# Performance work log

Measured on AMD Instinct MI355X. Metric: run time of the kernel, lower is better.

## Reference

```python
import jax, jax.numpy as jnp
import numpy as np

NEG_INF = -1e32

def _linear(x, W, b):
    # torch nn.Linear: x @ W.T + b
    return x @ W.T + b

def setup_inputs() -> dict:
    key = jax.random.key(0)
    B, T, D, H = 8, 1024, 512, 8
    ks = jax.random.split(key, 16)
    def rn(i, shape, scale=1.0):
        return jax.random.normal(ks[i], shape, dtype=jnp.float32) * scale
    W_SCALE = 0.04  # ~xavier for 512x512
    inp = {
        'q_mean': rn(0, (B, T, D)), 'q_cov': rn(1, (B, T, D)),
        'k_mean': rn(2, (B, T, D)), 'k_cov': rn(3, (B, T, D)),
        'v_mean': rn(4, (B, T, D)), 'v_cov': rn(5, (B, T, D)),
        # kq_same=True: q projections share k weights
        'Wk_mean': rn(6, (D, D), W_SCALE), 'bk_mean': jnp.zeros((D,), jnp.float32),
        'Wk_cov':  rn(7, (D, D), W_SCALE), 'bk_cov':  jnp.zeros((D,), jnp.float32),
        'Wv_mean': rn(8, (D, D), W_SCALE), 'bv_mean': jnp.zeros((D,), jnp.float32),
        'Wv_cov':  rn(9, (D, D), W_SCALE), 'bv_cov':  jnp.zeros((D,), jnp.float32),
        'Wo_mean': rn(10, (D, D), W_SCALE), 'bo_mean': jnp.zeros((D,), jnp.float32),
        'Wo_cov':  rn(11, (D, D), W_SCALE), 'bo_cov':  jnp.zeros((D,), jnp.float32),
        'gammas': rn(12, (H, 1, 1), 0.3),
        'mask': jnp.broadcast_to(jnp.tril(jnp.ones((T, T), dtype=bool))[None, None], (B, 1, T, T)),
        'zero_pad': 1,
    }
    return inp

def reference(q_mean, q_cov, k_mean, k_cov, v_mean, v_cov,
              Wk_mean, bk_mean, Wk_cov, bk_cov,
              Wv_mean, bv_mean, Wv_cov, bv_cov,
              Wo_mean, bo_mean, Wo_cov, bo_cov,
              gammas, mask, zero_pad):
    B, T, D = q_mean.shape
    H = gammas.shape[0]
    dk = D // H
    def split(x):  # (B,T,D) -> (B,H,T,dk)
        return x.reshape(B, T, H, dk).transpose(0, 2, 1, 3)
    km = split(_linear(k_mean, Wk_mean, bk_mean))
    kc = split(_linear(k_cov,  Wk_cov,  bk_cov))
    qm = split(_linear(q_mean, Wk_mean, bk_mean))  # kq_same
    qc = split(_linear(q_cov,  Wk_cov,  bk_cov))
    vm = split(_linear(v_mean, Wv_mean, bv_mean))
    vc = split(_linear(v_cov,  Wv_cov,  bv_cov))

    # Wasserstein distance (B,H,T,T)
    m1sq = jnp.sum(qm ** 2, -1, keepdims=True)
    m2sq = jnp.sum(km ** 2, -1, keepdims=True)
    ret = -2.0 * jnp.einsum('bhtd,bhsd->bhts', qm, km) + m1sq + jnp.swapaxes(m2sq, -1, -2)
    sq_q = jnp.sqrt(jnp.clip(qc, 1e-24))
    sq_k = jnp.sqrt(jnp.clip(kc, 1e-24))
    cov_ret = (-2.0 * jnp.einsum('bhtd,bhsd->bhts', sq_q, sq_k)
               + jnp.sum(qc, -1, keepdims=True)
               + jnp.swapaxes(jnp.sum(kc, -1, keepdims=True), -1, -2))
    scores = -(ret + cov_ret) / jnp.sqrt(jnp.float32(dk))

    # cumulative position-decay term (no-grad block in torch)
    s_ = jnp.where(mask, scores, NEG_INF)
    s_ = jax.nn.softmax(s_, axis=-1) * mask.astype(scores.dtype)
    distcum = jnp.cumsum(s_, axis=-1)
    disttot = jnp.sum(s_, axis=-1, keepdims=True)
    idx = jnp.arange(T)
    pos = jnp.abs(idx[None, :] - idx[:, None]).astype(jnp.float32)[None, None]  # (1,1,T,T)
    dist_scores = jax.lax.stop_gradient(jnp.sqrt(jnp.clip((disttot - distcum) * pos, 0.0)))

    gamma = -jax.nn.softplus(gammas)[None]  # (1,H,1,1)
    total_effect = jnp.clip(jnp.exp(dist_scores * gamma), 1e-5, 1e5)
    scores = jnp.where(mask, scores * total_effect, NEG_INF)
    scores = jax.nn.softmax(scores, axis=-1)
    if zero_pad:
        scores = scores.at[:, :, 0, :].set(0.0)
    # dropout is identity (p=0 / eval)

    out_mean = jnp.einsum('bhts,bhsd->bhtd', scores, vm)
    out_cov  = jnp.einsum('bhts,bhsd->bhtd', scores ** 2, vc)
    cm = out_mean.transpose(0, 2, 1, 3).reshape(B, T, D)
    cc = out_cov.transpose(0, 2, 1, 3).reshape(B, T, D)
    return (_linear(cm, Wo_mean, bo_mean), _linear(cc, Wo_cov, bo_cov))
```

## Files before the change

kernel.cpp:

```cpp
#include <hip/hip_runtime.h>
#include <hip/hip_bf16.h>
#include <hip/hip_fp16.h>

#define Bb 8
#define Tt 1024
#define Dd 512
#define Hh 8

typedef _Float16 half8 __attribute__((ext_vector_type(8)));
typedef float floatx4 __attribute__((ext_vector_type(4)));

__device__ __forceinline__ half8 cvt8(float4 a, float4 b) {
    half8 h;
    h[0] = (_Float16)a.x; h[1] = (_Float16)a.y; h[2] = (_Float16)a.z; h[3] = (_Float16)a.w;
    h[4] = (_Float16)b.x; h[5] = (_Float16)b.y; h[6] = (_Float16)b.z; h[7] = (_Float16)b.w;
    return h;
}

__device__ __forceinline__ void async16(const _Float16* g, _Float16* l) {
    __builtin_amdgcn_global_load_lds(
        (const __attribute__((address_space(1))) uint32_t*)g,
        (__attribute__((address_space(3))) uint32_t*)l, 16, 0, 0);
}

#define DPP_ADD(v, ctrl) \
    ((v) + __int_as_float(__builtin_amdgcn_update_dpp(0, __float_as_int(v), (ctrl), 0xF, 0xF, true)))

__device__ __forceinline__ float red16(float v) {
    v = DPP_ADD(v, 0xB1);
    v = DPP_ADD(v, 0x4E);
    v = DPP_ADD(v, 0x141);
    v = DPP_ADD(v, 0x140);
    return v;
}
__device__ __forceinline__ float scan16(float v) {
    v = DPP_ADD(v, 0x111);
    v = DPP_ADD(v, 0x112);
    v = DPP_ADD(v, 0x114);
    v = DPP_ADD(v, 0x118);
    return v;
}

__global__ __launch_bounds__(256) void cvt_pre(
    const float* __restrict__ s0, const float* __restrict__ s1,
    const float* __restrict__ s2, const float* __restrict__ s3,
    const float* __restrict__ s4, const float* __restrict__ s5,
    const float* __restrict__ w0, const float* __restrict__ w1,
    const float* __restrict__ w2, const float* __restrict__ w3,
    const float* __restrict__ w4, const float* __restrict__ w5,
    _Float16* __restrict__ dst)
{
    const size_t N_BTD = (size_t)Bb * Tt * Dd;
    const size_t NX = 6 * N_BTD;
    const size_t total8 = (NX + 6 * 262144) / 8;
    size_t i = (size_t)blockIdx.x * 256 + threadIdx.x;
    const size_t stride = (size_t)gridDim.x * 256;
    for (; i < total8; i += stride) {
        const size_t e = i * 8;
        const float* src;
        size_t off;
        if (e < NX) {
            const int seg = (int)(e >> 22);
            off = e & (N_BTD - 1);
            src = (seg == 0) ? s0 : (seg == 1) ? s1 : (seg == 2) ? s2
                : (seg == 3) ? s3 : (seg == 4) ? s4 : s5;
        } else {
            const size_t we = e - NX;
            const int seg = (int)(we >> 18);
            off = we & 262143;
            src = (seg == 0) ? w0 : (seg == 1) ? w1 : (seg == 2) ? w2
                : (seg == 3) ? w3 : (seg == 4) ? w4 : w5;
        }
        float4 a = *(const float4*)(src + off);
        float4 b = *(const float4*)(src + off + 4);
        *(half8*)(dst + e) = cvt8(a, b);
    }
}

template<bool TR>
__device__ __forceinline__ void gemm_tile_h(
    const _Float16* __restrict__ X, const _Float16* __restrict__ W,
    _Float16* As, _Float16* Bs, int m0, int n0, floatx4 acc[8])
{
    const int tid = threadIdx.x;
    const int w = tid >> 6, lane = tid & 63;
    const int sl = lane & 15, quad = lane >> 4;

    for (int k0 = 0; k0 < 512; k0 += 64) {
        __syncthreads();
        {
            const int r = tid >> 2;
            const int cb = (tid & 3) * 16;
            const _Float16* xp = X + (size_t)(m0 + r) * 512 + k0 + cb;
            *(uint4*)(As + r * 72 + cb)     = *(const uint4*)(xp);
            *(uint4*)(As + r * 72 + cb + 8) = *(const uint4*)(xp + 8);
        }
        {
            const int r = tid >> 1;
            const int cb = (tid & 1) * 32;
            const _Float16* wp = W + (size_t)(n0 + r) * 512 + k0 + cb;
            #pragma unroll
            for (int i = 0; i < 4; i++)
                *(uint4*)(Bs + r * 72 + cb + i * 8) = *(const uint4*)(wp + i * 8);
        }
        __syncthreads();
        #pragma unroll
        for (int kc = 0; kc < 64; kc += 32) {
            const half8 af = *(const half8*)(As + (w * 16 + sl) * 72 + kc + quad * 8);
            #pragma unroll
            for (int tn = 0; tn < 8; tn++) {
                const half8 bf = *(const half8*)(Bs + (tn * 16 + sl) * 72 + kc + quad * 8);
                if constexpr (TR)
                    acc[tn] = __builtin_amdgcn_mfma_f32_16x16x32_f16(bf, af, acc[tn], 0, 0, 0);
                else
                    acc[tn] = __builtin_amdgcn_mfma_f32_16x16x32_f16(af, bf, acc[tn], 0, 0, 0);
            }
        }
    }
}

__global__ __launch_bounds__(256) void gemm6(
    const _Float16* __restrict__ XH, const _Float16* __restrict__ WH,
    const float* __restrict__ bk_mean, const float* __restrict__ bk_cov,
    const float* __restrict__ bv_mean, const float* __restrict__ bv_cov,
    _Float16* __restrict__ QB, _Float16* __restrict__ KB, _Float16* __restrict__ VB,
    float* __restrict__ RROW, float* __restrict__ CCOL)
{
    __shared__ __align__(16) _Float16 As[64 * 72];
    __shared__ __align__(16) _Float16 Bs[128 * 72];

    const int f = blockIdx.x;
    const int work = (f & 7) * 384 + (f >> 3);
    const int z = work >> 9;
    const int rem = work & 511;
    const int m0 = (rem >> 2) * 64;
    const int n0 = (rem & 3) * 128;

    const size_t N_BTD = (size_t)Bb * Tt * Dd;
    const _Float16* X = XH + (size_t)z * N_BTD;
    const _Float16* W;
    const float* bias;
    _Float16* outH; float* sums;
    int off, sumsq, do_sqrt;
    switch (z) {
    case 0:  W=WH;            bias=bk_mean; outH=QB; sums=RROW;   off=0;  sumsq=1; do_sqrt=0; break;
    case 1:  W=WH+262144;     bias=bk_cov;  outH=QB; sums=RROW;   off=64; sumsq=0; do_sqrt=1; break;
    case 2:  W=WH;            bias=bk_mean; outH=KB; sums=CCOL;   off=0;  sumsq=1; do_sqrt=0; break;
    case 3:  W=WH+262144;     bias=bk_cov;  outH=KB; sums=CCOL;   off=64; sumsq=0; do_sqrt=1; break;
    case 4:  W=WH+2*262144;   bias=bv_mean; outH=VB; sums=nullptr;off=0;  sumsq=0; do_sqrt=0; break;
    default: W=WH+3*262144;   bias=bv_cov;  outH=VB; sums=nullptr;off=64; sumsq=0; do_sqrt=0; break;
    }

    floatx4 acc[8];
    #pragma unroll
    for (int tn = 0; tn < 8; tn++) acc[tn] = (floatx4){0.f, 0.f, 0.f, 0.f};

    const int tid = threadIdx.x;
    const int w = tid >> 6, lane = tid & 63;
    const int sl = lane & 15, quad = lane >> 4;

    if (z < 4) {
        gemm_tile_h<false>(X, W, As, Bs, m0, n0, acc);
        #pragma unroll
        for (int r = 0; r < 4; r++) {
            const int m = m0 + w * 16 + quad * 4 + r;
            const int b = m >> 10, t = m & 1023;
            float rs0 = 0.f, rs1 = 0.f;
            #pragma unroll
            for (int tn = 0; tn < 8; tn++) {
                const int n = n0 + tn * 16 + sl;
                const float v = acc[tn][r] + bias[n];
                if (tn < 4) rs0 += sumsq ? v * v : v;
                else        rs1 += sumsq ? v * v : v;
                const float sv = do_sqrt ? sqrtf(fmaxf(v, 1e-24f)) : v;
                const int head = n >> 6, dd = n & 63;
                outH[(((size_t)b * Hh + head) * Tt + t) * 128 + off + dd] = (_Float16)sv;
            }
            if (sums) {
                float v0 = rs0, v1 = rs1;
                v0 += __shfl_xor(v0, 1); v0 += __shfl_xor(v0, 2);
                v0 += __shfl_xor(v0, 4); v0 += __shfl_xor(v0, 8);
                v1 += __shfl_xor(v1, 1); v1 += __shfl_xor(v1, 2);
                v1 += __shfl_xor(v1, 4); v1 += __shfl_xor(v1, 8);
                if (sl == 0) {
                    atomicAdd(&sums[((size_t)b * Hh + (n0 >> 6) + 0) * Tt + t], v0);
                    atomicAdd(&sums[((size_t)b * Hh + (n0 >> 6) + 1) * Tt + t], v1);
                }
            }
        }
    } else {
        gemm_tile_h<true>(X, W, As, Bs, m0, n0, acc);
        const int m = m0 + w * 16 + sl;
        const int b = m >> 10, t = m & 1023;
        #pragma unroll
        for (int r = 0; r < 4; r++) {
            #pragma unroll
            for (int tn = 0; tn < 8; tn++) {
                const int n = n0 + tn * 16 + quad * 4 + r;
                const float v = acc[tn][r] + bias[n];
                const int head = n >> 6, dd = n & 63;
                outH[(((size_t)b * Hh + head) * 128 + off + dd) * 1024 + t] = (_Float16)v;
            }
        }
    }
}

__global__ __launch_bounds__(256) void gemm_out(
    const _Float16* __restrict__ CMh, const _Float16* __restrict__ CCh,
    const _Float16* __restrict__ WH,
    const float* __restrict__ bo_mean, const float* __restrict__ bo_cov,
    float* __restrict__ out, size_t outStride)
{
    __shared__ __align__(16) _Float16 As[64 * 72];
    __shared__ __align__(16) _Float16 Bs[128 * 72];

    const int f = blockIdx.x;
    const int work = (f & 7) * 128 + (f >> 3);
    const int z = work >> 9;
    const int rem = work & 511;
    const int m0 = (rem >> 2) * 64;
    const int n0 = (rem & 3) * 128;

    const _Float16* X = z ? CCh : CMh;
    const _Float16* W = WH + (size_t)(4 + z) * 262144;
    const float* bias = z ? bo_cov : bo_mean;
    float* outF       = out + (size_t)z * outStride;

    floatx4 acc[8];
    #pragma unroll
    for (int tn = 0; tn < 8; tn++) acc[tn] = (floatx4){0.f, 0.f, 0.f, 0.f};
    gemm_tile_h<false>(X, W, As, Bs, m0, n0, acc);

    const int tid = threadIdx.x;
    const int w = tid >> 6, lane = tid & 63;
    const int sl = lane & 15, quad = lane >> 4;

    #pragma unroll
    for (int r = 0; r < 4; r++) {
        const int m = m0 + w * 16 + quad * 4 + r;
        #pragma unroll
        for (int tn = 0; tn < 8; tn++) {
            const int n = n0 + tn * 16 + sl;
            outF[(size_t)m * 512 + n] = acc[tn][r] + bias[n];
        }
    }
}

__global__ __launch_bounds__(256) void attn_kernel(
    const _Float16* __restrict__ QB, const _Float16* __restrict__ KB,
    const _Float16* __restrict__ VBt, const float* __restrict__ RROW,
    const float* __restrict__ CCOL, const float* __restrict__ gammas,
    const int* __restrict__ zp, _Float16* __restrict__ CMh, _Float16* __restrict__ CCh)
{
    __shared__ __align__(16) _Float16 Vt[2][128 * 64];
    __shared__ __align__(16) _Float16 Pm[4][16 * 64];

    const int tid = threadIdx.x;
    const int g = blockIdx.x >> 6;
    const int bh = blockIdx.x & 63;
    const int rt = (g < 8) ? (15 - g) : (g - 8);
    const int t0 = rt * 64;
    const int h = bh & 7, b = bh >> 3;
    const int w = tid >> 6, lane = tid & 63;
    const int sl = lane & 15, quad = lane >> 4;
    const size_t rowbase = (size_t)bh * Tt;
    const int nch = rt + 1;

    const _Float16* VBb = VBt + (size_t)bh * 128 * 1024;
    const int vr8 = tid >> 3;
    const int vc8 = (tid & 7) << 3;
    const int vswz = (vr8 & 7) << 3;
    const _Float16* vsrc0 = VBb + (size_t)vr8 * 1024 + (vc8 ^ vswz);
    #define STAGE_V(cc, buf) do {                                          \
        const _Float16* _s = vsrc0 + (cc) * 64;                            \
        _Float16* _d = &Vt[(buf)][0] + vr8 * 64 + vc8;                     \
        _Pragma("unroll")                                                  \
        for (int _i = 0; _i < 4; _i++)                                     \
            async16(_s + (size_t)_i * 32 * 1024, _d + _i * 32 * 64);       \
    } while (0)

    STAGE_V(0, 0);

    half8 af[4];
    {
        const _Float16* qrow = QB + (rowbase + t0 + w * 16 + sl) * 128;
        #pragma unroll
        for (int ks = 0; ks < 4; ks++)
            af[ks] = *(const half8*)(qrow + ks * 32 + quad * 8);
    }

    const float gamma = -log1pf(__expf(gammas[h]));
    const int zero_pad = *zp;
    const int tbase = t0 + w * 16 + quad * 4;

    float rt_[4];
    #pragma unroll
    for (int r = 0; r < 4; r++) rt_[r] = RROW[rowbase + tbase + r];

    const _Float16* KBb = KB + rowbase * 128;
    const float* CCb = CCOL + rowbase;

    float l1p[4] = {0.f, 0.f, 0.f, 0.f};
    for (int c = 0; c < nch; ++c) {
        #pragma unroll
        for (int su = 0; su < 4; su++) {
            const int scol = c * 64 + su * 16 + sl;
            const _Float16* kr = KBb + (size_t)scol * 128;
            floatx4 acc = {0.f, 0.f, 0.f, 0.f};
            #pragma unroll
            for (int ks = 0; ks < 4; ks++) {
                half8 bf = *(const half8*)(kr + ks * 32 + quad * 8);
                acc = __builtin_amdgcn_mfma_f32_16x16x32_f16(af[ks], bf, acc, 0, 0, 0);
            }
            const float cs = CCb[scol];
            #pragma unroll
            for (int r = 0; r < 4; r++) {
                const float S = 0.25f * acc[r] - 0.125f * (rt_[r] + cs);
                l1p[r] += (scol <= tbase + r) ? __expf(S) : 0.f;
            }
        }
    }
    float invl1[4];
    #pragma unroll
    for (int r = 0; r < 4; r++) invl1[r] = 1.f / red16(l1p[r]);

    __syncthreads();

    float cumc[4] = {0.f, 0.f, 0.f, 0.f};
    float runL2[4] = {0.f, 0.f, 0.f, 0.f};
    floatx4 accm[4], accc[4];
    #pragma unroll
    for (int nt = 0; nt < 4; nt++) {
        accm[nt] = (floatx4){0.f, 0.f, 0.f, 0.f};
        accc[nt] = (floatx4){0.f, 0.f, 0.f, 0.f};
    }
    _Float16* PmW = &Pm[w][0];

    for (int c = 0; c < nch; ++c) {
        const int cur = c & 1;
        if (c + 1 < nch) STAGE_V(c + 1, cur ^ 1);

        float p2v[4][4];
        float csum[4] = {0.f, 0.f, 0.f, 0.f};
        #pragma unroll
        for (int su = 0; su < 4; su++) {
            const int scol = c * 64 + su * 16 + sl;
            const _Float16* kr = KBb + (size_t)scol * 128;
            floatx4 acc = {0.f, 0.f, 0.f, 0.f};
            #pragma unroll
            for (int ks = 0; ks < 4; ks++) {
                half8 bf = *(const half8*)(kr + ks * 32 + quad * 8);
                acc = __builtin_amdgcn_mfma_f32_16x16x32_f16(af[ks], bf, acc, 0, 0, 0);
            }
            const float cs = CCb[scol];
            #pragma unroll
            for (int r = 0; r < 4; r++) {
                const bool valid = (scol <= tbase + r);
                const float S = 0.25f * acc[r] - 0.125f * (rt_[r] + cs);
                const float p1 = valid ? __expf(S) : 0.f;
                const float cum = cumc[r] + scan16(p1);
                cumc[r] += red16(p1);
                const float sn = 1.f - cum * invl1[r];
                const float dsq = sn * (float)(tbase + r - scol);
                const float dist = sqrtf(fmaxf(dsq, 0.f));
                float dec = __expf(gamma * dist);
                dec = fminf(fmaxf(dec, 1e-5f), 1e5f);
                const float p2 = valid ? __expf(S * dec) : 0.f;
                p2v[su][r] = p2;
                csum[r] += p2;
            }
        }

        float invL2c[4];
        #pragma unroll
        for (int r = 0; r < 4; r++) {
            const float v = red16(csum[r]);
            const float newL2 = runL2[r] + v;
            const float inv = 1.f / newL2;
            const float ratio = runL2[r] * inv;
            runL2[r] = newL2;
            invL2c[r] = inv;
            const float ratio2 = ratio * ratio;
            #pragma unroll
            for (int nt = 0; nt < 4; nt++) {
                accm[nt][r] *= ratio;
                accc[nt][r] *= ratio2;
            }
        }
        #pragma unroll
        for (int su = 0; su < 4; su++) {
            #pragma unroll
            for (int r = 0; r < 4; r++) {
                const float pn = p2v[su][r] * invL2c[r];
                const int prow = quad * 4 + r;
                PmW[prow * 64 + ((su * 16 + sl) ^ ((prow & 7) << 3))] = (_Float16)pn;
            }
        }

        const _Float16* Vc = &Vt[cur][0];
        #pragma unroll
        for (int ks = 0; ks < 2; ks++) {
            const int kb = ks * 32 + quad * 8;
            half8 am = *(const half8*)(PmW + sl * 64 + (kb ^ ((sl & 7) << 3)));
            half8 ac = am * am;
            #pragma unroll
            for (int nt = 0; nt < 4; nt++) {
                const int rm = nt * 16 + sl, rc = rm + 64;
                half8 bm = *(const half8*)(Vc + rm * 64 + (kb ^ ((rm & 7) << 3)));
                half8 bc = *(const half8*)(Vc + rc * 64 + (kb ^ ((rc & 7) << 3)));
                accm[nt] = __builtin_amdgcn_mfma_f32_16x16x32_f16(am, bm, accm[nt], 0, 0, 0);
                accc[nt] = __builtin_amdgcn_mfma_f32_16x16x32_f16(ac, bc, accc[nt], 0, 0, 0);
            }
        }
        __syncthreads();
    }

    #pragma unroll
    for (int r = 0; r < 4; r++) {
        const int t = tbase + r;
        const bool zr = (zero_pad && t == 0);
        _Float16* cmp = CMh + ((size_t)b * Tt + t) * Dd + h * 64;
        _Float16* ccp = CCh + ((size_t)b * Tt + t) * Dd + h * 64;
        #pragma unroll
        for (int nt = 0; nt < 4; nt++) {
            const int d = nt * 16 + sl;
            cmp[d] = (_Float16)(zr ? 0.f : accm[nt][r]);
            ccp[d] = (_Float16)(zr ? 0.f : accc[nt][r]);
        }
    }
    #undef STAGE_V
}

extern "C" void kernel_launch(void* const* d_in, const int* in_sizes, int n_in,
                              void* d_out, int out_size, void* d_ws, size_t ws_size,
                              hipStream_t stream)
{
    const float* q_mean  = (const float*)d_in[0];
    const float* q_cov   = (const float*)d_in[1];
    const float* k_mean  = (const float*)d_in[2];
    const float* k_cov   = (const float*)d_in[3];
    const float* v_mean  = (const float*)d_in[4];
    const float* v_cov   = (const float*)d_in[5];
    const float* Wk_mean = (const float*)d_in[6];
    const float* bk_mean = (const float*)d_in[7];
    const float* Wk_cov  = (const float*)d_in[8];
    const float* bk_cov  = (const float*)d_in[9];
    const float* Wv_mean = (const float*)d_in[10];
    const float* bv_mean = (const float*)d_in[11];
    const float* Wv_cov  = (const float*)d_in[12];
    const float* bv_cov  = (const float*)d_in[13];
    const float* Wo_mean = (const float*)d_in[14];
    const float* bo_mean = (const float*)d_in[15];
    const float* Wo_cov  = (const float*)d_in[16];
    const float* bo_cov  = (const float*)d_in[17];
    const float* gammas  = (const float*)d_in[18];
    const int* zero_pad  = (const int*)d_in[20];
    float* out = (float*)d_out;

    const size_t N_BHT128 = (size_t)Bb * Hh * Tt * 128;
    const size_t N_BHT    = (size_t)Bb * Hh * Tt;
    const size_t N_BTD    = (size_t)Bb * Tt * Dd;

    const size_t needed = 3 * N_BHT128 * sizeof(_Float16)
                        + 6 * N_BTD * sizeof(_Float16)
                        + 6 * 262144 * sizeof(_Float16)
                        + 2 * N_BHT * sizeof(float);
    if (ws_size < needed) return;

    _Float16* QB = (_Float16*)d_ws;
    _Float16* KB = QB + N_BHT128;
    _Float16* VB = KB + N_BHT128;
    _Float16* XH = VB + N_BHT128;
    _Float16* WH = XH + 6 * N_BTD;
    float* RROW = (float*)(WH + 6 * 262144);
    float* CCOL = RROW + N_BHT;
    _Float16* CMh = XH;
    _Float16* CCh = CMh + N_BTD;

    hipMemsetAsync(RROW, 0, 2 * N_BHT * sizeof(float), stream);

    cvt_pre<<<dim3(2048), dim3(256), 0, stream>>>(
        q_mean, q_cov, k_mean, k_cov, v_mean, v_cov,
        Wk_mean, Wk_cov, Wv_mean, Wv_cov, Wo_mean, Wo_cov, XH);

    gemm6<<<dim3(3072), dim3(256), 0, stream>>>(
        XH, WH, bk_mean, bk_cov, bv_mean, bv_cov,
        QB, KB, VB, RROW, CCOL);

    attn_kernel<<<dim3(1024), dim3(256), 0, stream>>>(
        QB, KB, VB, RROW, CCOL, gammas, zero_pad, CMh, CCh);

    gemm_out<<<dim3(1024), dim3(256), 0, stream>>>(
        CMh, CCh, WH, bo_mean, bo_cov, out, N_BTD);
}
```

Measured before the change: 482.4 us.

## Split softmax-denominator pass into separate triangular-tiled kernel with atomics

The first-pass row-sum of exp scores, previously computed serially per row-tile inside the attention kernel, moves into its own kernel. That kernel launches one block per (row tile, column chunk) pair over the causal triangle and accumulates partial sums into a global L1 buffer with atomics. The main attention kernel then reads the precomputed denominators. This spreads the load-imbalanced first pass across many more blocks, at the cost of an extra launch, recomputing Q fragment loads, and atomic traffic.

```diff
diff --git a/kernel.cpp b/kernel.cpp
--- a/kernel.cpp
+++ b/kernel.cpp
@@ -246,11 +246,70 @@
     }
 }
 
-__global__ __launch_bounds__(256) void attn_kernel(
+__global__ __launch_bounds__(256) void pass_a(
+    const _Float16* __restrict__ QB, const _Float16* __restrict__ KB,
+    const float* __restrict__ RROW, const float* __restrict__ CCOL,
+    float* __restrict__ L1)
+{
+    const int tri = blockIdx.x;
+    int rt = (int)((sqrtf(8.f * (float)tri + 1.f) - 1.f) * 0.5f);
+    while ((rt + 1) * (rt + 2) / 2 <= tri) rt++;
+    while (rt * (rt + 1) / 2 > tri) rt--;
+    const int c = tri - rt * (rt + 1) / 2;
+    const int bh = blockIdx.y;
+
+    const int tid = threadIdx.x;
+    const int w = tid >> 6, lane = tid & 63;
+    const int sl = lane & 15, quad = lane >> 4;
+    const int t0 = rt * 64;
+    const int tbase = t0 + w * 16 + quad * 4;
+    const size_t rowbase = (size_t)bh * Tt;
+
+    half8 af[4];
+    {
+        const _Float16* qrow = QB + (rowbase + t0 + w * 16 + sl) * 128;
+        #pragma unroll
+        for (int ks = 0; ks < 4; ks++)
+            af[ks] = *(const half8*)(qrow + ks * 32 + quad * 8);
+    }
+    float rt_[4];
+    #pragma unroll
+    for (int r = 0; r < 4; r++) rt_[r] = RROW[rowbase + tbase + r];
+
+    const _Float16* KBb = KB + rowbase * 128;
+    const float* CCb = CCOL + rowbase;
+
+    float l1p[4] = {0.f, 0.f, 0.f, 0.f};
+    #pragma unroll
+    for (int su = 0; su < 4; su++) {
+        const int scol = c * 64 + su * 16 + sl;
+        const _Float16* kr = KBb + (size_t)scol * 128;
+        floatx4 acc = {0.f, 0.f, 0.f, 0.f};
+        #pragma unroll
+        for (int ks = 0; ks < 4; ks++) {
+            half8 bf = *(const half8*)(kr + ks * 32 + quad * 8);
+            acc = __builtin_amdgcn_mfma_f32_16x16x32_f16(af[ks], bf, acc, 0, 0, 0);
+        }
+        const float cs = CCb[scol];
+        #pragma unroll
+        for (int r = 0; r < 4; r++) {
+            const float S = 0.25f * acc[r] - 0.125f * (rt_[r] + cs);
+            l1p[r] += (scol <= tbase + r) ? __expf(S) : 0.f;
+        }
+    }
+    #pragma unroll
+    for (int r = 0; r < 4; r++) {
+        const float v = red16(l1p[r]);
+        if (sl == 0) atomicAdd(&L1[rowbase + tbase + r], v);
+    }
+}
+
+__global__ __launch_bounds__(256) void attn_b(
     const _Float16* __restrict__ QB, const _Float16* __restrict__ KB,
     const _Float16* __restrict__ VBt, const float* __restrict__ RROW,
-    const float* __restrict__ CCOL, const float* __restrict__ gammas,
-    const int* __restrict__ zp, _Float16* __restrict__ CMh, _Float16* __restrict__ CCh)
+    const float* __restrict__ CCOL, const float* __restrict__ L1,
+    const float* __restrict__ gammas, const int* __restrict__ zp,
+    _Float16* __restrict__ CMh, _Float16* __restrict__ CCh)
 {
     __shared__ __align__(16) _Float16 Vt[2][128 * 64];
     __shared__ __align__(16) _Float16 Pm[4][16 * 64];
@@ -293,36 +352,15 @@
     const int zero_pad = *zp;
     const int tbase = t0 + w * 16 + quad * 4;
 
-    float rt_[4];
-    #pragma unroll
-    for (int r = 0; r < 4; r++) rt_[r] = RROW[rowbase + tbase + r];
+    float rt_[4], invl1[4];
+    #pragma unroll
+    for (int r = 0; r < 4; r++) {
+        rt_[r] = RROW[rowbase + tbase + r];
+        invl1[r] = 1.f / L1[rowbase + tbase + r];
+    }
 
     const _Float16* KBb = KB + rowbase * 128;
     const float* CCb = CCOL + rowbase;
-
-    float l1p[4] = {0.f, 0.f, 0.f, 0.f};
-    for (int c = 0; c < nch; ++c) {
-        #pragma unroll
-        for (int su = 0; su < 4; su++) {
-            const int scol = c * 64 + su * 16 + sl;
-            const _Float16* kr = KBb + (size_t)scol * 128;
-            floatx4 acc = {0.f, 0.f, 0.f, 0.f};
-            #pragma unroll
-            for (int ks = 0; ks < 4; ks++) {
-                half8 bf = *(const half8*)(kr + ks * 32 + quad * 8);
-                acc = __builtin_amdgcn_mfma_f32_16x16x32_f16(af[ks], bf, acc, 0, 0, 0);
-            }
-            const float cs = CCb[scol];
-            #pragma unroll
-            for (int r = 0; r < 4; r++) {
-                const float S = 0.25f * acc[r] - 0.125f * (rt_[r] + cs);
-                l1p[r] += (scol <= tbase + r) ? __expf(S) : 0.f;
-            }
-        }
-    }
-    float invl1[4];
-    #pragma unroll
-    for (int r = 0; r < 4; r++) invl1[r] = 1.f / red16(l1p[r]);
 
     __syncthreads();
 
@@ -464,7 +502,7 @@
     const size_t needed = 3 * N_BHT128 * sizeof(_Float16)
                         + 6 * N_BTD * sizeof(_Float16)
                         + 6 * 262144 * sizeof(_Float16)
-                        + 2 * N_BHT * sizeof(float);
+                        + 3 * N_BHT * sizeof(float);
     if (ws_size < needed) return;
 
     _Float16* QB = (_Float16*)d_ws;
@@ -474,10 +512,11 @@
     _Float16* WH = XH + 6 * N_BTD;
     float* RROW = (float*)(WH + 6 * 262144);
     float* CCOL = RROW + N_BHT;
+    float* L1   = CCOL + N_BHT;
     _Float16* CMh = XH;
     _Float16* CCh = CMh + N_BTD;
 
-    hipMemsetAsync(RROW, 0, 2 * N_BHT * sizeof(float), stream);
+    hipMemsetAsync(RROW, 0, 3 * N_BHT * sizeof(float), stream);
 
     cvt_pre<<<dim3(2048), dim3(256), 0, stream>>>(
         q_mean, q_cov, k_mean, k_cov, v_mean, v_cov,
@@ -487,8 +526,11 @@
         XH, WH, bk_mean, bk_cov, bv_mean, bv_cov,
         QB, KB, VB, RROW, CCOL);
 
-    attn_kernel<<<dim3(1024), dim3(256), 0, stream>>>(
-        QB, KB, VB, RROW, CCOL, gammas, zero_pad, CMh, CCh);
+    pass_a<<<dim3(136, 64), dim3(256), 0, stream>>>(
+        QB, KB, RROW, CCOL, L1);
+
+    attn_b<<<dim3(1024), dim3(256), 0, stream>>>(
+        QB, KB, VB, RROW, CCOL, L1, gammas, zero_pad, CMh, CCh);
 
     gemm_out<<<dim3(1024), dim3(256), 0, stream>>>(
         CMh, CCh, WH, bo_mean, bo_cov, out, N_BTD);
```

Result: no change. 487.6 us (+1.1%).
